# Optimization experiments

Hardware: AMD Instinct MI355X
Metric: run time of the kernel (lower is better)

## Reference

```python
import jax, jax.numpy as jnp
import numpy as np

NDIM = (256, 256, 256)
NMIN = (-1.0, -1.0, -1.0)
NMAX = (1.0, 1.0, 1.0)
NDELTA = tuple((NMAX[i] - NMIN[i]) / (NDIM[i] - 1.0) for i in range(3))
MIN_DEG, MAX_DEG = 0, 10
ANNEALED_ALPHA = 1.0
EPS = 1e-12


def compute_grad(grid):
    # central differences on the voxel grid with edge padding -> [N, 3]
    g = grid.reshape(NDIM[0], NDIM[1], NDIM[2])
    p = jnp.pad(g, ((1, 1), (1, 1), (1, 1)), mode='edge')
    dx = (p[2:, 1:-1, 1:-1] - p[:-2, 1:-1, 1:-1]) / (2.0 * NDELTA[0])
    dy = (p[1:-1, 2:, 1:-1] - p[1:-1, :-2, 1:-1]) / (2.0 * NDELTA[1])
    dz = (p[1:-1, 1:-1, 2:] - p[1:-1, 1:-1, :-2]) / (2.0 * NDELTA[2])
    return jnp.stack([dx, dy, dz], axis=-1).reshape(-1, 3)


def trilinear3(data, pts):
    # data: [N, 4] flattened voxel features, pts: [B, 3] -> [B, 4]
    x = (pts[..., 0] - NMIN[0]) / NDELTA[0]
    y = (pts[..., 1] - NMIN[1]) / NDELTA[1]
    z = (pts[..., 2] - NMIN[2]) / NDELTA[2]
    x0f = jnp.floor(x); y0f = jnp.floor(y); z0f = jnp.floor(z)
    xd = (x - x0f)[..., None]
    yd = (y - y0f)[..., None]
    zd = (z - z0f)[..., None]
    x0 = jnp.clip(x0f.astype(jnp.int32), 0, NDIM[0] - 1)
    x1 = jnp.clip(x0f.astype(jnp.int32) + 1, 0, NDIM[0] - 1)
    y0 = jnp.clip(y0f.astype(jnp.int32), 0, NDIM[1] - 1)
    y1 = jnp.clip(y0f.astype(jnp.int32) + 1, 0, NDIM[1] - 1)
    z0 = jnp.clip(z0f.astype(jnp.int32), 0, NDIM[2] - 1)
    z1 = jnp.clip(z0f.astype(jnp.int32) + 1, 0, NDIM[2] - 1)
    sYZ, sZ = NDIM[1] * NDIM[2], NDIM[2]
    gat = lambda i, j, k: data[sYZ * i + sZ * j + k]
    c00 = gat(x0, y0, z0) * (1 - xd) + gat(x1, y0, z0) * xd
    c01 = gat(x0, y0, z1) * (1 - xd) + gat(x1, y0, z1) * xd
    c10 = gat(x0, y1, z0) * (1 - xd) + gat(x1, y1, z0) * xd
    c11 = gat(x0, y1, z1) * (1 - xd) + gat(x1, y1, z1) * xd
    c0 = c00 * (1 - yd) + c10 * yd
    c1 = c01 * (1 - yd) + c11 * yd
    return c0 * (1 - zd) + c1 * zd


def annealed_pos_enc(x, alpha):
    # nerfies-style windowed positional encoding with identity concat
    bands = jnp.arange(MIN_DEG, MAX_DEG, dtype=x.dtype)  # [D]
    scales = 2.0 ** bands
    xb = x[..., None, :] * scales[:, None]               # [..., D, 3]
    four = jnp.sin(jnp.stack([xb, xb + 0.5 * jnp.pi], axis=-2))  # [..., D, 2, 3]
    w = jnp.clip(alpha - bands, 0.0, 1.0)
    w = 0.5 * (1.0 - jnp.cos(jnp.pi * w))                # cosine easing window
    four = four * w[:, None, None]
    four = four.reshape(x.shape[:-1] + (-1,))            # [..., D*6]
    return jnp.concatenate([x, four], axis=-1)           # [..., 3 + D*6]


def mlp(feats, w0, b0, w1, b1, w2, b2, w3, b3, wo, bo):
    # net_depth=4, skip_layer=2 -> concat inputs after layer index 2
    h = jax.nn.relu(feats @ w0 + b0)
    h = jax.nn.relu(h @ w1 + b1)
    h = jax.nn.relu(h @ w2 + b2)
    h = jnp.concatenate([h, feats], axis=-1)
    h = jax.nn.relu(h @ w3 + b3)
    return h @ wo + bo


def safe_l2_norm(v):
    return jnp.sqrt(jnp.sum(v * v, axis=-1, keepdims=True) + EPS)


def setup_inputs() -> dict:
    key = jax.random.key(0)
    ks = jax.random.split(key, 8)
    B = 1048576
    N = NDIM[0] * NDIM[1] * NDIM[2]
    x = jax.random.uniform(ks[0], (B, 3), jnp.float32, -1.0, 1.0)
    grid = jax.random.normal(ks[1], (N, 1), jnp.float32)
    glorot = lambda k, fi, fo: jax.random.normal(k, (fi, fo), jnp.float32) * jnp.sqrt(2.0 / (fi + fo))
    return {
        'x': x, 'grid': grid,
        'w0': glorot(ks[2], 63, 128), 'b0': jnp.zeros((128,), jnp.float32),
        'w1': glorot(ks[3], 128, 128), 'b1': jnp.zeros((128,), jnp.float32),
        'w2': glorot(ks[4], 128, 128), 'b2': jnp.zeros((128,), jnp.float32),
        'w3': glorot(ks[5], 191, 128), 'b3': jnp.zeros((128,), jnp.float32),
        'wo': jax.random.normal(ks[6], (128, 3), jnp.float32) * 1e-5,  # output_init normal(1e-5)
        'bo': jnp.zeros((3,), jnp.float32),
    }


def reference(x, grid, w0, b0, w1, b1, w2, b2, w3, b3, wo, bo):
    data = jnp.concatenate([grid, compute_grad(grid)], axis=-1)  # [N, 4]
    ret = trilinear3(data, x)                                    # [B, 4]
    feats = annealed_pos_enc(x[:, None], ANNEALED_ALPHA * MAX_DEG)  # [B, 1, 63]
    raw = mlp(feats, w0, b0, w1, b1, w2, b2, w3, b3, wo, bo)[:, 0]  # [B, 3]
    # residual + direct output: rotate gradient vector by axis-angle raw
    theta = safe_l2_norm(raw)
    e = raw / theta
    cond = ret[..., 1:]
    a = safe_l2_norm(cond)
    v = cond / a
    rot = a * (jnp.cos(theta) * v + jnp.sin(theta) * jnp.cross(e, v)
               + (1.0 - jnp.cos(theta)) * jnp.sum(e * v, axis=-1, keepdims=True) * e)
    return (ret[..., :1], ret[..., 1:], rot)
```

## Files before the change

kernel.cpp:

```cpp
#include <hip/hip_runtime.h>


typedef __attribute__((ext_vector_type(4))) float f4;
typedef long long llg;
typedef __attribute__((ext_vector_type(2))) long long llg2;
typedef unsigned long long u64;

#define MFMA8 __builtin_amdgcn_mfma_f32_16x16x32_fp8_fp8
#define SCHED_FENCE() __builtin_amdgcn_sched_barrier(0)

__device__ __forceinline__ float bf2f(unsigned int u) {
    union { float f; unsigned int i; } v; v.i = u << 16; return v.f;
}
__device__ __forceinline__ unsigned int pkbf(float a, float b) {
    unsigned int r;
    asm("v_cvt_pk_bf16_f32 %0, %1, %2" : "=v"(r) : "v"(a), "v"(b));
    return r;
}
__device__ __forceinline__ float vfract(float a) {
    float d; asm("v_fract_f32 %0, %1" : "=v"(d) : "v"(a)); return d;
}
__device__ __forceinline__ float vsin(float a) {
    float d; asm("v_sin_f32 %0, %1" : "=v"(d) : "v"(a)); return d;
}
__device__ __forceinline__ float gv(const float* __restrict__ g, int i, int j, int k) {
    return g[(i * 256 + j) * 256 + k];
}
__device__ __forceinline__ int featmap(int kp) {
    if (kp < 3) return kp;
    if (kp == 3) return -1;
    const int m = kp - 4, b = m / 6, r = m - 6 * b, d = r >> 1, c = r & 1;
    return 3 + 6 * b + 3 * c + d;
}
__device__ __forceinline__ int hidperm(int k) {
    const int kt = k >> 5, q = (k >> 3) & 3, j = k & 7;
    return 32 * kt + ((j >> 2) << 4) + (q << 2) + (j & 3);
}
__device__ __forceinline__ llg mkllg(unsigned int lo, unsigned int hi) {
    return (llg)(((unsigned long long)lo) | (((unsigned long long)hi) << 32));
}
__device__ __forceinline__ unsigned int pack8(f4 acc) {
    int d = __builtin_amdgcn_cvt_pk_fp8_f32(fmaxf(acc[0], 0.f), fmaxf(acc[1], 0.f), 0, false);
    d     = __builtin_amdgcn_cvt_pk_fp8_f32(fmaxf(acc[2], 0.f), fmaxf(acc[3], 0.f), d, true);
    return (unsigned int)d;
}

#define WS_TOTAL 67584
#define SWZ_BLOCKS 264
#define DG_BLOCKS 8192
#define DG_OFF_SH 131072
#define WS_NEED (262144ull + 16777216ull * 8ull)
#define WO_SCALE 8192.0f
#define WO_INV   (1.0f / 8192.0f)
#define INV2PI 0.15915494309189535f

__global__ __launch_bounds__(256) void prep(
    const float* __restrict__ g,
    const float* __restrict__ w0, const float* __restrict__ w1,
    const float* __restrict__ w2, const float* __restrict__ w3,
    const float* __restrict__ wo,
    unsigned char* __restrict__ ws8, unsigned short* __restrict__ dg,
    int do_dgrid)
{
    const int bid = blockIdx.x;
    if (bid < SWZ_BLOCKS) {
        int idx = bid * 256 + threadIdx.x;
        const float* src; int base, KTP, Kact, Nact, ld;
        if (idx < 8192)       { src = w0; base = 0;     KTP = 1; Kact = 64;  Nact = 128; ld = 128; }
        else if (idx < 24576) { src = w1; base = 8192;  KTP = 2; Kact = 128; Nact = 128; ld = 128; }
        else if (idx < 40960) { src = w2; base = 24576; KTP = 2; Kact = 128; Nact = 128; ld = 128; }
        else if (idx < 65536) { src = w3; base = 40960; KTP = 3; Kact = 192; Nact = 128; ld = 128; }
        else                  { src = wo; base = 65536; KTP = 2; Kact = 128; Nact = 3;   ld = 3;   }
        int local = idx - base;
        int j    = local & 7;
        int half = (local >> 3) & 1;
        int lane = (local >> 4) & 63;
        int c    = local >> 10;
        int ktp  = c % KTP, nt = c / KTP;
        int kt   = ktp * 2 + half;
        int k = kt * 32 + ((lane >> 4) << 3) + j;
        int n = nt * 16 + (lane & 15);
        float v = 0.0f;
        if (k < Kact && n < Nact) {
            int ko;
            if (base == 0) {
                ko = featmap(k);
            } else if (base == 40960) {
                if (k >= 128) {
                    int f = featmap(k - 128);
                    ko = (f < 0) ? -1 : 128 + f;
                } else {
                    ko = hidperm(k);
                }
            } else {
                ko = hidperm(k);
            }
            if (ko >= 0) v = src[ko * ld + n];
            if (base == 65536) v *= WO_SCALE;
        }
        int p = __builtin_amdgcn_cvt_pk_fp8_f32(v, v, 0, false);
        ws8[idx] = (unsigned char)(p & 0xff);
    } else if (do_dgrid) {
        const int t  = (bid - SWZ_BLOCKS) * 256 + threadIdx.x;
        const int k0 = (t & 31) << 3;
        const int j  = (t >> 5) & 255;
        const int i  = t >> 13;
        const float* row = g + (i * 256 + j) * 256;
        const float* rxp = g + (min(i + 1, 255) * 256 + j) * 256;
        const float* rxm = g + (max(i - 1, 0)   * 256 + j) * 256;
        const float* ryp = g + (i * 256 + min(j + 1, 255)) * 256;
        const float* rym = g + (i * 256 + max(j - 1, 0))   * 256;
        float se[8], sxp[8], sxm[8], syp[8], sym[8];
        {
            f4 a = *(const f4*)(row + k0), b = *(const f4*)(row + k0 + 4);
            #pragma unroll
            for (int q = 0; q < 4; ++q) { se[q] = a[q]; se[q + 4] = b[q]; }
            a = *(const f4*)(rxp + k0); b = *(const f4*)(rxp + k0 + 4);
            #pragma unroll
            for (int q = 0; q < 4; ++q) { sxp[q] = a[q]; sxp[q + 4] = b[q]; }
            a = *(const f4*)(rxm + k0); b = *(const f4*)(rxm + k0 + 4);
            #pragma unroll
            for (int q = 0; q < 4; ++q) { sxm[q] = a[q]; sxm[q + 4] = b[q]; }
            a = *(const f4*)(ryp + k0); b = *(const f4*)(ryp + k0 + 4);
            #pragma unroll
            for (int q = 0; q < 4; ++q) { syp[q] = a[q]; syp[q + 4] = b[q]; }
            a = *(const f4*)(rym + k0); b = *(const f4*)(rym + k0 + 4);
            #pragma unroll
            for (int q = 0; q < 4; ++q) { sym[q] = a[q]; sym[q + 4] = b[q]; }
        }
        float zv[10];
        zv[0] = row[max(k0 - 1, 0)];
        #pragma unroll
        for (int q = 0; q < 8; ++q) zv[q + 1] = se[q];
        zv[9] = row[min(k0 + 8, 255)];
        unsigned int o[16];
        #pragma unroll
        for (int q = 0; q < 8; ++q) {
            o[q * 2 + 0] = pkbf(se[q], (sxp[q] - sxm[q]) * 63.75f);
            o[q * 2 + 1] = pkbf((syp[q] - sym[q]) * 63.75f, (zv[q + 2] - zv[q]) * 63.75f);
        }
        unsigned short* dst = dg + (size_t)(((i * 256 + j) * 256 + k0)) * 4;
        #pragma unroll
        for (int q = 0; q < 4; ++q)
            *(uint4*)(dst + q * 8) = *(const uint4*)(&o[q * 4]);
    }
}

#define FSTRIDE_B 88
#define WV_BYTES (32 * FSTRIDE_B)

#define HIDDEN_LAYER(WSL, BIASP, SRCP, DSTP)                                    \
    do {                                                                        \
        _Pragma("unroll")                                                       \
        for (int utp = 0; utp < 4; ++utp) {                                     \
            const int utA = 2 * utp, utB = 2 * utp + 1;                         \
            llg2 wa0 = *(const llg2*)((WSL) + ((utA * 2 + 0) * 64 + lane) * 16);\
            llg2 wa1 = *(const llg2*)((WSL) + ((utA * 2 + 1) * 64 + lane) * 16);\
            llg2 wb0 = *(const llg2*)((WSL) + ((utB * 2 + 0) * 64 + lane) * 16);\
            llg2 wb1 = *(const llg2*)((WSL) + ((utB * 2 + 1) * 64 + lane) * 16);\
            const f4 biasA = *(const f4*)((BIASP) + utA * 16 + quad * 4);       \
            const f4 biasB = *(const f4*)((BIASP) + utB * 16 + quad * 4);       \
            _Pragma("unroll")                                                   \
            for (int pt = 0; pt < 2; ++pt) {                                    \
                f4 a0 = biasA, a1 = biasB;                                      \
                a0 = MFMA8(wa0[0], SRCP[pt][0], a0, 0, 0, 0);                   \
                a0 = MFMA8(wa0[1], SRCP[pt][1], a0, 0, 0, 0);                   \
                a0 = MFMA8(wa1[0], SRCP[pt][2], a0, 0, 0, 0);                   \
                a0 = MFMA8(wa1[1], SRCP[pt][3], a0, 0, 0, 0);                   \
                a1 = MFMA8(wb0[0], SRCP[pt][0], a1, 0, 0, 0);                   \
                a1 = MFMA8(wb0[1], SRCP[pt][1], a1, 0, 0, 0);                   \
                a1 = MFMA8(wb1[0], SRCP[pt][2], a1, 0, 0, 0);                   \
                a1 = MFMA8(wb1[1], SRCP[pt][3], a1, 0, 0, 0);                   \
                DSTP[pt][utp] = mkllg(pack8(a0), pack8(a1));                    \
            }                                                                   \
            SCHED_FENCE();                                                      \
        }                                                                       \
    } while (0)

template<bool FAST>
__global__ __launch_bounds__(256, 5) void voxmlp(
    const float* __restrict__ x, const float* __restrict__ grid,
    const unsigned char* __restrict__ ws8, const unsigned short* __restrict__ dg,
    const float* __restrict__ b0, const float* __restrict__ b1,
    const float* __restrict__ b2, const float* __restrict__ b3,
    const float* __restrict__ bo,
    float* __restrict__ out, int B)
{
    __shared__ unsigned char smem[WV_BYTES * 4];

    const int lane = threadIdx.x & 63;
    const int wave = threadIdx.x >> 6;
    const int quad = lane >> 4;
    const int lm   = lane & 15;
    unsigned char* fbuf = smem + wave * WV_BYTES;

    const int pbase = blockIdx.x * 128 + wave * 32;

    const int p2   = lane & 31;
    const int role = lane >> 5;
    const int pid  = pbase + p2;

    const float px = x[pid * 3 + 0];
    const float py = x[pid * 3 + 1];
    const float pz = x[pid * 3 + 2];

    if (FAST) {
        const float fx = (px + 1.0f) * 127.5f;
        const float fy = (py + 1.0f) * 127.5f;
        const float fz = (pz + 1.0f) * 127.5f;
        const float fx0 = floorf(fx), fy0 = floorf(fy), fz0 = floorf(fz);
        const float xd = fx - fx0, yd = fy - fy0, zd = fz - fz0;
        const int ix0 = min(max((int)fx0, 0), 255);
        const int iy0 = min(max((int)fy0, 0), 255);
        const int iz0 = min(max((int)fz0, 0), 255);
        const int ix1 = min(ix0 + 1, 255);
        const int iy1 = min(iy0 + 1, 255);
        const int iz1 = min(iz0 + 1, 255);

        const unsigned char* dgb = (const unsigned char*)dg;
        const unsigned int vbase = (unsigned int)((ix0 * 65536 + iy0 * 256 + iz0) << 3);
        const unsigned int ox = (unsigned int)((ix1 - ix0) << 19);
        const unsigned int oy = (unsigned int)((iy1 - iy0) << 11);
        const unsigned int oz = (unsigned int)((iz1 - iz0) << 3);

        u64 gl[8];
        #pragma unroll
        for (int c = 0; c < 8; ++c) {
            const unsigned int off = vbase + ((c & 4) ? ox : 0u)
                                           + ((c & 2) ? oy : 0u)
                                           + ((c & 1) ? oz : 0u);
            gl[c] = *(const u64*)(dgb + off);
        }
        #pragma unroll
        for (int c = 0; c < 8; ++c)
            asm volatile("" : "+v"(gl[c]));

        if (role == 1) {
            const float r0 = px * INV2PI, r1 = py * INV2PI, r2 = pz * INV2PI;
            unsigned char* fb = fbuf + p2 * FSTRIDE_B;
            auto slotv = [&](int n) -> float {
                if (n == 0) return px;
                if (n == 1) return py;
                if (n == 2) return pz;
                if (n == 3) return 0.0f;
                const int m = n - 4, b = m / 6, t = m % 6, ax = t >> 1, ph = t & 1;
                const float rr = (ax == 0) ? r0 : (ax == 1) ? r1 : r2;
                const float arg = rr * (float)(1 << b) + (ph ? 0.25f : 0.0f);
                return vsin(vfract(arg));
            };
            #pragma unroll
            for (int w = 0; w < 8; ++w) {
                int lo = __builtin_amdgcn_cvt_pk_fp8_f32(slotv(8 * w + 0), slotv(8 * w + 1), 0, false);
                lo     = __builtin_amdgcn_cvt_pk_fp8_f32(slotv(8 * w + 2), slotv(8 * w + 3), lo, true);
                int hi = __builtin_amdgcn_cvt_pk_fp8_f32(slotv(8 * w + 4), slotv(8 * w + 5), 0, false);
                hi     = __builtin_amdgcn_cvt_pk_fp8_f32(slotv(8 * w + 6), slotv(8 * w + 7), hi, true);
                uint2 pk; pk.x = (unsigned int)lo; pk.y = (unsigned int)hi;
                *(uint2*)(fb + w * 8) = pk;
            }
        } else {
            float ret0 = 0.f, c1 = 0.f, c2 = 0.f, c3 = 0.f;
            #pragma unroll
            for (int c = 0; c < 8; ++c) {
                const float wgt = ((c & 4) ? xd : 1.0f - xd) *
                                  ((c & 2) ? yd : 1.0f - yd) *
                                  ((c & 1) ? zd : 1.0f - zd);
                const unsigned int wx = (unsigned int)gl[c];
                const unsigned int wy = (unsigned int)(gl[c] >> 32);
                ret0 = fmaf(wgt, bf2f(wx & 0xffffu), ret0);
                c1   = fmaf(wgt, bf2f(wx >> 16),     c1);
                c2   = fmaf(wgt, bf2f(wy & 0xffffu), c2);
                c3   = fmaf(wgt, bf2f(wy >> 16),     c3);
            }
            out[pid] = ret0;
            out[B + pid * 3 + 0] = c1;
            out[B + pid * 3 + 1] = c2;
            out[B + pid * 3 + 2] = c3;
            float* cst = (float*)(fbuf + p2 * FSTRIDE_B + 64);
            cst[0] = c1; cst[1] = c2; cst[2] = c3;
        }
    } else {
        if (role == 0) {
            const float fx = (px + 1.0f) * 127.5f;
            const float fy = (py + 1.0f) * 127.5f;
            const float fz = (pz + 1.0f) * 127.5f;
            const float fx0 = floorf(fx), fy0 = floorf(fy), fz0 = floorf(fz);
            const float xd = fx - fx0, yd = fy - fy0, zd = fz - fz0;
            const int ix0 = min(max((int)fx0, 0), 255);
            const int iy0 = min(max((int)fy0, 0), 255);
            const int iz0 = min(max((int)fz0, 0), 255);
            const int ix1 = min(ix0 + 1, 255);
            const int iy1 = min(iy0 + 1, 255);
            const int iz1 = min(iz0 + 1, 255);
            float ret0 = 0.f, c1 = 0.f, c2 = 0.f, c3 = 0.f;
            #pragma unroll
            for (int c = 0; c < 8; ++c) {
                const int i = (c & 4) ? ix1 : ix0;
                const int j = (c & 2) ? iy1 : iy0;
                const int k = (c & 1) ? iz1 : iz0;
                const float wgt = ((c & 4) ? xd : 1.0f - xd) *
                                  ((c & 2) ? yd : 1.0f - yd) *
                                  ((c & 1) ? zd : 1.0f - zd);
                const float v  = gv(grid, i, j, k);
                const float gx = (gv(grid, min(i + 1, 255), j, k) - gv(grid, max(i - 1, 0), j, k)) * 63.75f;
                const float gy = (gv(grid, i, min(j + 1, 255), k) - gv(grid, i, max(j - 1, 0), k)) * 63.75f;
                const float gz = (gv(grid, i, j, min(k + 1, 255)) - gv(grid, i, j, max(k - 1, 0))) * 63.75f;
                ret0 = fmaf(wgt, v,  ret0);
                c1   = fmaf(wgt, gx, c1);
                c2   = fmaf(wgt, gy, c2);
                c3   = fmaf(wgt, gz, c3);
            }
            out[pid] = ret0;
            out[B + pid * 3 + 0] = c1;
            out[B + pid * 3 + 1] = c2;
            out[B + pid * 3 + 2] = c3;
            float* cst = (float*)(fbuf + p2 * FSTRIDE_B + 64);
            cst[0] = c1; cst[1] = c2; cst[2] = c3;
        } else {
            const float r0 = px * INV2PI, r1 = py * INV2PI, r2 = pz * INV2PI;
            unsigned char* fb = fbuf + p2 * FSTRIDE_B;
            auto slotv = [&](int n) -> float {
                if (n == 0) return px;
                if (n == 1) return py;
                if (n == 2) return pz;
                if (n == 3) return 0.0f;
                const int m = n - 4, b = m / 6, t = m % 6, ax = t >> 1, ph = t & 1;
                const float rr = (ax == 0) ? r0 : (ax == 1) ? r1 : r2;
                const float arg = rr * (float)(1 << b) + (ph ? 0.25f : 0.0f);
                return vsin(vfract(arg));
            };
            #pragma unroll
            for (int w = 0; w < 8; ++w) {
                int lo = __builtin_amdgcn_cvt_pk_fp8_f32(slotv(8 * w + 0), slotv(8 * w + 1), 0, false);
                lo     = __builtin_amdgcn_cvt_pk_fp8_f32(slotv(8 * w + 2), slotv(8 * w + 3), lo, true);
                int hi = __builtin_amdgcn_cvt_pk_fp8_f32(slotv(8 * w + 4), slotv(8 * w + 5), 0, false);
                hi     = __builtin_amdgcn_cvt_pk_fp8_f32(slotv(8 * w + 6), slotv(8 * w + 7), hi, true);
                uint2 pk; pk.x = (unsigned int)lo; pk.y = (unsigned int)hi;
                *(uint2*)(fb + w * 8) = pk;
            }
        }
    }
    __builtin_amdgcn_s_barrier();

    const int frow0 = lm * FSTRIDE_B + quad * 8;

    llg actA[2][4];
    llg actB[2][4];
    llg ffp[2][2];

    #pragma unroll
    for (int pt = 0; pt < 2; ++pt)
        #pragma unroll
        for (int kt = 0; kt < 2; ++kt)
            ffp[pt][kt] = *(const llg*)(fbuf + pt * 16 * FSTRIDE_B + frow0 + kt * 32);

    #pragma unroll
    for (int utp = 0; utp < 4; ++utp) {
        const int utA = 2 * utp, utB = 2 * utp + 1;
        llg2 wA = *(const llg2*)(ws8 + (utA * 64 + lane) * 16);
        llg2 wB = *(const llg2*)(ws8 + (utB * 64 + lane) * 16);
        const f4 biasA = *(const f4*)(b0 + utA * 16 + quad * 4);
        const f4 biasB = *(const f4*)(b0 + utB * 16 + quad * 4);
        #pragma unroll
        for (int pt = 0; pt < 2; ++pt) {
            f4 a0 = biasA, a1 = biasB;
            a0 = MFMA8(wA[0], ffp[pt][0], a0, 0, 0, 0);
            a0 = MFMA8(wA[1], ffp[pt][1], a0, 0, 0, 0);
            a1 = MFMA8(wB[0], ffp[pt][0], a1, 0, 0, 0);
            a1 = MFMA8(wB[1], ffp[pt][1], a1, 0, 0, 0);
            actA[pt][utp] = mkllg(pack8(a0), pack8(a1));
        }
        SCHED_FENCE();
    }

    HIDDEN_LAYER(ws8 + 8192,  b1, actA, actB);
    HIDDEN_LAYER(ws8 + 24576, b2, actB, actA);

    #pragma unroll
    for (int utp = 0; utp < 4; ++utp) {
        const int utA = 2 * utp, utB = 2 * utp + 1;
        llg2 ha0 = *(const llg2*)(ws8 + 40960 + ((utA * 3 + 0) * 64 + lane) * 16);
        llg2 ha1 = *(const llg2*)(ws8 + 40960 + ((utA * 3 + 1) * 64 + lane) * 16);
        llg2 ha2 = *(const llg2*)(ws8 + 40960 + ((utA * 3 + 2) * 64 + lane) * 16);
        llg2 hb0 = *(const llg2*)(ws8 + 40960 + ((utB * 3 + 0) * 64 + lane) * 16);
        llg2 hb1 = *(const llg2*)(ws8 + 40960 + ((utB * 3 + 1) * 64 + lane) * 16);
        llg2 hb2 = *(const llg2*)(ws8 + 40960 + ((utB * 3 + 2) * 64 + lane) * 16);
        const f4 biasA = *(const f4*)(b3 + utA * 16 + quad * 4);
        const f4 biasB = *(const f4*)(b3 + utB * 16 + quad * 4);
        #pragma unroll
        for (int pt = 0; pt < 2; ++pt) {
            f4 a0 = biasA, a1 = biasB;
            a0 = MFMA8(ha0[0], actA[pt][0], a0, 0, 0, 0);
            a0 = MFMA8(ha0[1], actA[pt][1], a0, 0, 0, 0);
            a0 = MFMA8(ha1[0], actA[pt][2], a0, 0, 0, 0);
            a0 = MFMA8(ha1[1], actA[pt][3], a0, 0, 0, 0);
            a0 = MFMA8(ha2[0], ffp[pt][0],  a0, 0, 0, 0);
            a0 = MFMA8(ha2[1], ffp[pt][1],  a0, 0, 0, 0);
            a1 = MFMA8(hb0[0], actA[pt][0], a1, 0, 0, 0);
            a1 = MFMA8(hb0[1], actA[pt][1], a1, 0, 0, 0);
            a1 = MFMA8(hb1[0], actA[pt][2], a1, 0, 0, 0);
            a1 = MFMA8(hb1[1], actA[pt][3], a1, 0, 0, 0);
            a1 = MFMA8(hb2[0], ffp[pt][0],  a1, 0, 0, 0);
            a1 = MFMA8(hb2[1], ffp[pt][1],  a1, 0, 0, 0);
            actB[pt][utp] = mkllg(pack8(a0), pack8(a1));
        }
        SCHED_FENCE();
    }

    const llg2 o0 = *(const llg2*)(ws8 + 65536 + (lane * 16));
    const llg2 o1 = *(const llg2*)(ws8 + 65536 + ((64 + lane) * 16));

    const float bo0 = bo[0], bo1 = bo[1], bo2 = bo[2];
    #pragma unroll
    for (int pt = 0; pt < 2; ++pt) {
        f4 acc = {0.f, 0.f, 0.f, 0.f};
        acc = MFMA8(o0[0], actB[pt][0], acc, 0, 0, 0);
        acc = MFMA8(o0[1], actB[pt][1], acc, 0, 0, 0);
        acc = MFMA8(o1[0], actB[pt][2], acc, 0, 0, 0);
        acc = MFMA8(o1[1], actB[pt][3], acc, 0, 0, 0);

        const int pp = pt * 16 + lm;
        const float* cst = (const float*)(fbuf + pp * FSTRIDE_B + 64);
        const float g1 = cst[0], g2 = cst[1], g3 = cst[2];
        const float r0 = acc[0] * WO_INV + bo0;
        const float r1 = acc[1] * WO_INV + bo1;
        const float r2 = acc[2] * WO_INV + bo2;
        const float theta = sqrtf(fmaf(r0, r0, fmaf(r1, r1, r2 * r2)) + 1e-12f);
        const float it = __builtin_amdgcn_rcpf(theta);
        const float e0 = r0 * it, e1 = r1 * it, e2 = r2 * it;
        const float a = sqrtf(fmaf(g1, g1, fmaf(g2, g2, g3 * g3)) + 1e-12f);
        const float ia = __builtin_amdgcn_rcpf(a);
        const float v0 = g1 * ia, v1 = g2 * ia, v2 = g3 * ia;
        const float rv = theta * INV2PI;
        const float st = vsin(vfract(rv));
        const float ct = vsin(vfract(rv + 0.25f));
        const float cx = e1 * v2 - e2 * v1;
        const float cy = e2 * v0 - e0 * v2;
        const float cz = e0 * v1 - e1 * v0;
        const float om = (1.0f - ct) * (e0 * v0 + e1 * v1 + e2 * v2);
        if (quad == 0) {
            const int pid2 = pbase + pp;
            out[4 * B + pid2 * 3 + 0] = a * (ct * v0 + st * cx + om * e0);
            out[4 * B + pid2 * 3 + 1] = a * (ct * v1 + st * cy + om * e1);
            out[4 * B + pid2 * 3 + 2] = a * (ct * v2 + st * cz + om * e2);
        }
    }
}

extern "C" void kernel_launch(void* const* d_in, const int* in_sizes, int n_in,
                              void* d_out, int out_size, void* d_ws, size_t ws_size,
                              hipStream_t stream)
{
    const float* x    = (const float*)d_in[0];
    const float* grid = (const float*)d_in[1];
    const float* w0   = (const float*)d_in[2];
    const float* b0   = (const float*)d_in[3];
    const float* w1   = (const float*)d_in[4];
    const float* b1   = (const float*)d_in[5];
    const float* w2   = (const float*)d_in[6];
    const float* b2   = (const float*)d_in[7];
    const float* w3   = (const float*)d_in[8];
    const float* b3   = (const float*)d_in[9];
    const float* wo   = (const float*)d_in[10];
    const float* bo   = (const float*)d_in[11];
    float* out = (float*)d_out;
    unsigned char* ws8 = (unsigned char*)d_ws;
    unsigned short* dg = (unsigned short*)d_ws + DG_OFF_SH;

    const int B = in_sizes[0] / 3;
    const int fast = (ws_size >= WS_NEED) ? 1 : 0;
    const int nprep = fast ? (SWZ_BLOCKS + DG_BLOCKS) : SWZ_BLOCKS;
    prep<<<nprep, 256, 0, stream>>>(grid, w0, w1, w2, w3, wo, ws8, dg, fast);
    if (fast)
        voxmlp<true><<<B / 128, 256, 0, stream>>>(x, grid, ws8, dg, b0, b1, b2, b3, bo, out, B);
    else
        voxmlp<false><<<B / 128, 256, 0, stream>>>(x, grid, ws8, dg, b0, b1, b2, b3, bo, out, B);
}
```

Before: 316.5 us.

## Store gradient grid in 2x2x2 bricked layout to improve gather locality

After: 374.2 us. 1.18x slower.

```diff
diff --git a/kernel.cpp b/kernel.cpp
--- a/kernel.cpp
+++ b/kernel.cpp
@@ -25,6 +25,11 @@
 }
 __device__ __forceinline__ float gv(const float* __restrict__ g, int i, int j, int k) {
     return g[(i * 256 + j) * 256 + k];
+}
+__device__ __forceinline__ void load8(float* d, const float* __restrict__ p) {
+    f4 a = *(const f4*)p, b = *(const f4*)(p + 4);
+    #pragma unroll
+    for (int q = 0; q < 4; ++q) { d[q] = a[q]; d[q + 4] = b[q]; }
 }
 __device__ __forceinline__ int featmap(int kp) {
     if (kp < 3) return kp;
@@ -44,10 +49,19 @@
     d     = __builtin_amdgcn_cvt_pk_fp8_f32(fmaxf(acc[2], 0.f), fmaxf(acc[3], 0.f), d, true);
     return (unsigned int)d;
 }
+__device__ __forceinline__ unsigned int ax_(int x) {
+    return ((unsigned int)(x >> 1) << 20) + ((unsigned int)(x & 1) << 5);
+}
+__device__ __forceinline__ unsigned int ay_(int y) {
+    return ((unsigned int)(y >> 1) << 13) + ((unsigned int)(y & 1) << 4);
+}
+__device__ __forceinline__ unsigned int az_(int z) {
+    return ((unsigned int)(z >> 1) << 6) + ((unsigned int)(z & 1) << 3);
+}
 
 #define WS_TOTAL 67584
 #define SWZ_BLOCKS 264
-#define DG_BLOCKS 8192
+#define DG_BLOCKS 2048
 #define DG_OFF_SH 131072
 #define WS_NEED (262144ull + 16777216ull * 8ull)
 #define WO_SCALE 8192.0f
@@ -102,47 +116,64 @@
         ws8[idx] = (unsigned char)(p & 0xff);
     } else if (do_dgrid) {
         const int t  = (bid - SWZ_BLOCKS) * 256 + threadIdx.x;
-        const int k0 = (t & 31) << 3;
-        const int j  = (t >> 5) & 255;
-        const int i  = t >> 13;
-        const float* row = g + (i * 256 + j) * 256;
-        const float* rxp = g + (min(i + 1, 255) * 256 + j) * 256;
-        const float* rxm = g + (max(i - 1, 0)   * 256 + j) * 256;
-        const float* ryp = g + (i * 256 + min(j + 1, 255)) * 256;
-        const float* rym = g + (i * 256 + max(j - 1, 0))   * 256;
-        float se[8], sxp[8], sxm[8], syp[8], sym[8];
-        {
-            f4 a = *(const f4*)(row + k0), b = *(const f4*)(row + k0 + 4);
+        const int kc = t & 31;
+        const int j0 = (t >> 5) & 127;
+        const int i0 = t >> 12;
+        const int k0 = kc << 3;
+        const int x0 = 2 * i0, x1 = x0 + 1;
+        const int y0 = 2 * j0, y1 = y0 + 1;
+        const int xm = max(x0 - 1, 0), xp = min(x1 + 1, 255);
+        const int ym = max(y0 - 1, 0), yp = min(y1 + 1, 255);
+
+        const float* pc00 = g + (x0 * 256 + y0) * 256 + k0;
+        const float* pc01 = g + (x0 * 256 + y1) * 256 + k0;
+        const float* pc10 = g + (x1 * 256 + y0) * 256 + k0;
+        const float* pc11 = g + (x1 * 256 + y1) * 256 + k0;
+        const float* pxm0 = g + (xm * 256 + y0) * 256 + k0;
+        const float* pxm1 = g + (xm * 256 + y1) * 256 + k0;
+        const float* pxp0 = g + (xp * 256 + y0) * 256 + k0;
+        const float* pxp1 = g + (xp * 256 + y1) * 256 + k0;
+        const float* pym0 = g + (x0 * 256 + ym) * 256 + k0;
+        const float* pym1 = g + (x1 * 256 + ym) * 256 + k0;
+        const float* pyp0 = g + (x0 * 256 + yp) * 256 + k0;
+        const float* pyp1 = g + (x1 * 256 + yp) * 256 + k0;
+
+        float a00[10], a01[10], a10[10], a11[10];
+        load8(a00 + 1, pc00); load8(a01 + 1, pc01);
+        load8(a10 + 1, pc10); load8(a11 + 1, pc11);
+        const bool lo = (k0 == 0), hi = (k0 == 248);
+        a00[0] = lo ? pc00[0] : pc00[-1]; a00[9] = hi ? pc00[7] : pc00[8];
+        a01[0] = lo ? pc01[0] : pc01[-1]; a01[9] = hi ? pc01[7] : pc01[8];
+        a10[0] = lo ? pc10[0] : pc10[-1]; a10[9] = hi ? pc10[7] : pc10[8];
+        a11[0] = lo ? pc11[0] : pc11[-1]; a11[9] = hi ? pc11[7] : pc11[8];
+        float hxm0[8], hxm1[8], hxp0[8], hxp1[8];
+        float hym0[8], hym1[8], hyp0[8], hyp1[8];
+        load8(hxm0, pxm0); load8(hxm1, pxm1);
+        load8(hxp0, pxp0); load8(hxp1, pxp1);
+        load8(hym0, pym0); load8(hym1, pym1);
+        load8(hyp0, pyp0); load8(hyp1, pyp1);
+
+        unsigned short* dstb = dg + ((size_t)((i0 * 128 + j0) * 128 + (k0 >> 1)) << 5);
+        #pragma unroll
+        for (int zb = 0; zb < 4; ++zb) {
+            unsigned int o[16];
             #pragma unroll
-            for (int q = 0; q < 4; ++q) { se[q] = a[q]; se[q + 4] = b[q]; }
-            a = *(const f4*)(rxp + k0); b = *(const f4*)(rxp + k0 + 4);
+            for (int dk = 0; dk < 2; ++dk) {
+                const int z = 1 + 2 * zb + dk;
+                const int h = z - 1;
+                o[0 + dk * 2] = pkbf(a00[z], (a10[z] - hxm0[h]) * 63.75f);
+                o[1 + dk * 2] = pkbf((a01[z] - hym0[h]) * 63.75f, (a00[z + 1] - a00[z - 1]) * 63.75f);
+                o[4 + dk * 2] = pkbf(a01[z], (a11[z] - hxm1[h]) * 63.75f);
+                o[5 + dk * 2] = pkbf((hyp0[h] - a00[z]) * 63.75f, (a01[z + 1] - a01[z - 1]) * 63.75f);
+                o[8 + dk * 2] = pkbf(a10[z], (hxp0[h] - a00[z]) * 63.75f);
+                o[9 + dk * 2] = pkbf((a11[z] - hym1[h]) * 63.75f, (a10[z + 1] - a10[z - 1]) * 63.75f);
+                o[12 + dk * 2] = pkbf(a11[z], (hxp1[h] - a01[z]) * 63.75f);
+                o[13 + dk * 2] = pkbf((hyp1[h] - a10[z]) * 63.75f, (a11[z + 1] - a11[z - 1]) * 63.75f);
+            }
             #pragma unroll
-            for (int q = 0; q < 4; ++q) { sxp[q] = a[q]; sxp[q + 4] = b[q]; }
-            a = *(const f4*)(rxm + k0); b = *(const f4*)(rxm + k0 + 4);
-            #pragma unroll
-            for (int q = 0; q < 4; ++q) { sxm[q] = a[q]; sxm[q + 4] = b[q]; }
-            a = *(const f4*)(ryp + k0); b = *(const f4*)(ryp + k0 + 4);
-            #pragma unroll
-            for (int q = 0; q < 4; ++q) { syp[q] = a[q]; syp[q + 4] = b[q]; }
-            a = *(const f4*)(rym + k0); b = *(const f4*)(rym + k0 + 4);
-            #pragma unroll
-            for (int q = 0; q < 4; ++q) { sym[q] = a[q]; sym[q + 4] = b[q]; }
-        }
-        float zv[10];
-        zv[0] = row[max(k0 - 1, 0)];
-        #pragma unroll
-        for (int q = 0; q < 8; ++q) zv[q + 1] = se[q];
-        zv[9] = row[min(k0 + 8, 255)];
-        unsigned int o[16];
-        #pragma unroll
-        for (int q = 0; q < 8; ++q) {
-            o[q * 2 + 0] = pkbf(se[q], (sxp[q] - sxm[q]) * 63.75f);
-            o[q * 2 + 1] = pkbf((syp[q] - sym[q]) * 63.75f, (zv[q + 2] - zv[q]) * 63.75f);
-        }
-        unsigned short* dst = dg + (size_t)(((i * 256 + j) * 256 + k0)) * 4;
-        #pragma unroll
-        for (int q = 0; q < 4; ++q)
-            *(uint4*)(dst + q * 8) = *(const uint4*)(&o[q * 4]);
+            for (int q = 0; q < 4; ++q)
+                *(uint4*)(dstb + zb * 32 + q * 8) = *(const uint4*)(&o[q * 4]);
+        }
     }
 }
 
@@ -218,10 +249,10 @@
         const int iz1 = min(iz0 + 1, 255);
 
         const unsigned char* dgb = (const unsigned char*)dg;
-        const unsigned int vbase = (unsigned int)((ix0 * 65536 + iy0 * 256 + iz0) << 3);
-        const unsigned int ox = (unsigned int)((ix1 - ix0) << 19);
-        const unsigned int oy = (unsigned int)((iy1 - iy0) << 11);
-        const unsigned int oz = (unsigned int)((iz1 - iz0) << 3);
+        const unsigned int vbase = ax_(ix0) + ay_(iy0) + az_(iz0);
+        const unsigned int ox = ax_(ix1) - ax_(ix0);
+        const unsigned int oy = ay_(iy1) - ay_(iy0);
+        const unsigned int oz = az_(iz1) - az_(iz0);
 
         u64 gl[8];
         #pragma unroll
```
